# Kernel tuning notes

Measured on AMD Instinct MI355X. Metric: run time of the kernel, lower is better.

## Reference

```python
import jax, jax.numpy as jnp
import numpy as np

B, L, DM = 1, 512, 768
DS, DC, EX = 64, 4, 2
DI = EX * DM            # d_inner = 1536
DR = DM // 16           # dt_rank = 48


def setup_inputs() -> dict:
    key = jax.random.key(0)
    ks = jax.random.split(key, 12)
    s = 0.02
    inp = {
        "x": jax.random.normal(ks[0], (B, L, DM), dtype=jnp.float32),
        "ln_w": jnp.ones((DM,), jnp.float32),
        "ln_b": jnp.zeros((DM,), jnp.float32),
        "in_proj_w": jax.random.normal(ks[1], (2 * DI, DM), jnp.float32) * s,
        "conv_w": jax.random.normal(ks[2], (DI, 1, DC), jnp.float32) * s,
        "conv_b": jnp.zeros((DI,), jnp.float32),
        "x_proj_w": jax.random.normal(ks[3], (DR + 2 * DS, DI), jnp.float32) * s,
        "dt_proj_w": jax.random.normal(ks[4], (DI, DR), jnp.float32) * s,
        "dt_proj_b": jax.random.normal(ks[5], (DI,), jnp.float32) * s,
        "A_log": jnp.log(jnp.broadcast_to(jnp.arange(1, DS + 1, dtype=jnp.float32), (DI, DS))),
        "D": jnp.ones((DI,), jnp.float32),
        "out_proj_w": jax.random.normal(ks[6], (DM, DI), jnp.float32) * s,
    }
    return inp


def _layernorm(x, w, b, eps=1e-5):
    mu = jnp.mean(x, axis=-1, keepdims=True)
    var = jnp.mean((x - mu) ** 2, axis=-1, keepdims=True)
    return (x - mu) * jax.lax.rsqrt(var + eps) * w + b


def _causal_depthwise_conv(x, w, b):
    # x: [B, L, DI] -> conv over time, depthwise, causal (left pad DC-1)
    xc = jnp.transpose(x, (0, 2, 1))  # [B, DI, L]
    y = jax.lax.conv_general_dilated(
        xc, w, window_strides=(1,), padding=[(DC - 1, 0)],
        dimension_numbers=("NCH", "OIH", "NCH"), feature_group_count=DI)
    y = y + b[None, :, None]
    return jnp.transpose(y, (0, 2, 1))  # [B, L, DI]


def _selective_scan(deltaA, deltaB_u, C):
    # deltaA, deltaB_u: [B, L, DI, DS]; C: [B, L, DS]
    dA = jnp.transpose(deltaA, (1, 0, 2, 3))
    dBu = jnp.transpose(deltaB_u, (1, 0, 2, 3))
    Ct = jnp.transpose(C, (1, 0, 2))
    s0 = jnp.zeros(deltaA.shape[:1] + deltaA.shape[2:], deltaA.dtype).transpose(0, 1, 2)
    s0 = jnp.zeros((deltaA.shape[0], deltaA.shape[2], deltaA.shape[3]), deltaA.dtype)

    def step(s, inp):
        dA_t, dBu_t, C_t = inp
        s = dA_t * s + dBu_t                      # [B, DI, DS]
        y = jnp.einsum("bdn,bn->bd", s, C_t)      # [B, DI]
        return s, y

    _, ys = jax.lax.scan(step, s0, (dA, dBu, Ct))
    return jnp.transpose(ys, (1, 0, 2))           # [B, L, DI]


def reference(x, ln_w, ln_b, in_proj_w, conv_w, conv_b, x_proj_w,
              dt_proj_w, dt_proj_b, A_log, D, out_proj_w):
    residual = x
    h = _layernorm(x, ln_w, ln_b)
    xz = jnp.einsum("bld,ed->ble", h, in_proj_w)  # [B, L, 2*DI]
    x_in, z = jnp.split(xz, 2, axis=-1)
    x_in = jax.nn.silu(_causal_depthwise_conv(x_in, conv_w, conv_b))
    x_dbl = jnp.einsum("bld,ed->ble", x_in, x_proj_w)  # [B, L, DR+2*DS]
    dt, Bm, Cm = jnp.split(x_dbl, [DR, DR + DS], axis=-1)
    dt = jax.nn.softplus(jnp.einsum("blr,dr->bld", dt, dt_proj_w) + dt_proj_b)  # [B,L,DI]
    A = -jnp.exp(A_log)                                 # [DI, DS]
    deltaA = jnp.exp(dt[..., None] * A)                 # [B, L, DI, DS]
    deltaB_u = dt[..., None] * Bm[:, :, None, :] * x_in[..., None]
    y = _selective_scan(deltaA, deltaB_u, Cm)           # [B, L, DI]
    y = y + x_in * D
    y = y * jax.nn.silu(z)
    out = jnp.einsum("bld,ed->ble", y, out_proj_w)      # [B, L, DM]
    return residual + out
```

## Files before the change

### kernel.cpp

```cpp
#include <hip/hip_runtime.h>
#include <hip/hip_bf16.h>
#include <math.h>

#define L_SEQ 512
#define DM 768
#define DI 1536
#define DS 64
#define DC 4
#define DR 48
#define NBC 128
#define NP2 (NBC + DI)
#define NC 8
#define TC 64

typedef __attribute__((ext_vector_type(8))) short short8;
typedef __attribute__((ext_vector_type(4))) float float4v;

#define J_LN 512
#define J_WI (2 * DI * DM / 1024)
#define J_WBC (NBC * DI / 1024)
#define J_WO (DM * DI / 1024)
#define J_WEFF ((DI / 64) * (DI / 64))
#define PREP_GRID (J_LN + J_WI + J_WBC + J_WO + J_WEFF)

__device__ __forceinline__ float bp_add(float p, int addr) {
  return p + __int_as_float(__builtin_amdgcn_ds_bpermute(addr, __float_as_int(p)));
}
__device__ __forceinline__ float lane_read(float v, int t) {
  return __int_as_float(__builtin_amdgcn_readlane(__float_as_int(v), t));
}
__device__ __forceinline__ short f2bf(float v) {
  __hip_bfloat16 h = __float2bfloat16(v);
  return *reinterpret_cast<short*>(&h);
}
__device__ __forceinline__ short8 cvt8f(const float* p, bool valid) {
  float4 u = *(const float4*)(p);
  float4 v = *(const float4*)(p + 4);
  short8 r;
  r[0] = f2bf(u.x); r[1] = f2bf(u.y); r[2] = f2bf(u.z); r[3] = f2bf(u.w);
  r[4] = f2bf(v.x); r[5] = f2bf(v.y); r[6] = f2bf(v.z); r[7] = f2bf(v.w);
  if (!valid) r = (short8)0;
  return r;
}
__device__ __forceinline__ void cvt_blk(const float* __restrict__ s,
                                        short* __restrict__ d, int b) {
  int i = b * 1024 + threadIdx.x * 4;
  float4 v = *(const float4*)(s + i);
  short4 o; o.x = f2bf(v.x); o.y = f2bf(v.y); o.z = f2bf(v.z); o.w = f2bf(v.w);
  *(short4*)(d + i) = o;
}

__device__ __forceinline__ float4v gemm32_core(
    const short* __restrict__ A, int lda, const short* __restrict__ B, int ldb,
    int K, int bx, int by, int lane, int w, float4v* red,
    int* prow, int* pcol) {
  int ks = K >> 2;
  int kbeg = w * ks;
  int fr = lane & 15, koff = (lane >> 4) * 8;
  int m0 = by * 32, n0 = bx * 32;
  const short* pA0 = A + (size_t)(m0 + fr) * lda + koff + kbeg;
  const short* pA1 = pA0 + (size_t)16 * lda;
  const short* pB0 = B + (size_t)(n0 + fr) * ldb + koff + kbeg;
  const short* pB1 = pB0 + (size_t)16 * ldb;
  float4v acc00 = (float4v){0.f,0.f,0.f,0.f}, acc01 = acc00;
  float4v acc10 = acc00, acc11 = acc00;
  short8 a0A = *(const short8*)(pA0);      short8 a1A = *(const short8*)(pA1);
  short8 b0A = *(const short8*)(pB0);      short8 b1A = *(const short8*)(pB1);
  short8 a0B = *(const short8*)(pA0 + 32); short8 a1B = *(const short8*)(pA1 + 32);
  short8 b0B = *(const short8*)(pB0 + 32); short8 b1B = *(const short8*)(pB1 + 32);
  for (int k0 = 0; k0 < ks; k0 += 64) {
    short8 ca0 = a0A, ca1 = a1A, cb0 = b0A, cb1 = b1A;
    short8 da0 = a0B, da1 = a1B, db0 = b0B, db1 = b1B;
    int nA = k0 + 64; if (nA >= ks) nA = 0;
    int nB = k0 + 96; if (nB >= ks) nB = 32;
    a0A = *(const short8*)(pA0 + nA); a1A = *(const short8*)(pA1 + nA);
    b0A = *(const short8*)(pB0 + nA); b1A = *(const short8*)(pB1 + nA);
    a0B = *(const short8*)(pA0 + nB); a1B = *(const short8*)(pA1 + nB);
    b0B = *(const short8*)(pB0 + nB); b1B = *(const short8*)(pB1 + nB);
    acc00 = __builtin_amdgcn_mfma_f32_16x16x32_bf16(ca0, cb0, acc00, 0, 0, 0);
    acc01 = __builtin_amdgcn_mfma_f32_16x16x32_bf16(ca0, cb1, acc01, 0, 0, 0);
    acc10 = __builtin_amdgcn_mfma_f32_16x16x32_bf16(ca1, cb0, acc10, 0, 0, 0);
    acc11 = __builtin_amdgcn_mfma_f32_16x16x32_bf16(ca1, cb1, acc11, 0, 0, 0);
    acc00 = __builtin_amdgcn_mfma_f32_16x16x32_bf16(da0, db0, acc00, 0, 0, 0);
    acc01 = __builtin_amdgcn_mfma_f32_16x16x32_bf16(da0, db1, acc01, 0, 0, 0);
    acc10 = __builtin_amdgcn_mfma_f32_16x16x32_bf16(da1, db0, acc10, 0, 0, 0);
    acc11 = __builtin_amdgcn_mfma_f32_16x16x32_bf16(da1, db1, acc11, 0, 0, 0);
  }
  red[(w * 4 + 0) * 64 + lane] = acc00;
  red[(w * 4 + 1) * 64 + lane] = acc01;
  red[(w * 4 + 2) * 64 + lane] = acc10;
  red[(w * 4 + 3) * 64 + lane] = acc11;
  __syncthreads();
  float4v v = red[(0 * 4 + w) * 64 + lane];
  v = v + red[(1 * 4 + w) * 64 + lane];
  v = v + red[(2 * 4 + w) * 64 + lane];
  v = v + red[(3 * 4 + w) * 64 + lane];
  int qi = w & 1, qj = w >> 1;
  *prow = m0 + qi * 16 + (lane >> 4) * 4;
  *pcol = n0 + qj * 16 + (lane & 15);
  return v;
}

__global__ __launch_bounds__(256) void prep(
    const float* __restrict__ x, const float* __restrict__ lnw,
    const float* __restrict__ lnb, short* __restrict__ h,
    const float* __restrict__ wi, short* __restrict__ wib,
    const float* __restrict__ wx, const float* __restrict__ wdt,
    short* __restrict__ wcomb, const float* __restrict__ wo,
    short* __restrict__ wob) {
  __shared__ float ls[4], ls2[4];
  int b = blockIdx.x;
  int tid = threadIdx.x, lane = tid & 63, w = tid >> 6;
  if (b < J_LN) {
    int l = b;
    const float* xr = x + l * DM;
    float s = 0.f, s2 = 0.f;
    for (int i = tid; i < DM; i += 256) { float t = xr[i]; s += t; s2 += t * t; }
#pragma unroll
    for (int off = 32; off; off >>= 1) { s += __shfl_xor(s, off); s2 += __shfl_xor(s2, off); }
    if (lane == 0) { ls[w] = s; ls2[w] = s2; }
    __syncthreads();
    s = ls[0] + ls[1] + ls[2] + ls[3];
    s2 = ls2[0] + ls2[1] + ls2[2] + ls2[3];
    float mean = s * (1.f / DM);
    float var = s2 * (1.f / DM) - mean * mean;
    float rstd = rsqrtf(var + 1e-5f);
    for (int i = tid; i < DM; i += 256)
      h[l * DM + i] = f2bf((xr[i] - mean) * rstd * lnw[i] + lnb[i]);
    return;
  }
  b -= J_LN;
  if (b < J_WI) { cvt_blk(wi, wib, b); return; }
  b -= J_WI;
  if (b < J_WBC) { cvt_blk(wx + DR * DI, wcomb, b); return; }
  b -= J_WBC;
  if (b < J_WO) { cvt_blk(wo, wob, b); return; }
  b -= J_WO;
  {
    int tm = b / (DI / 64), tn = b % (DI / 64);
    int qi = w & 1, qj = w >> 1;
    int m0 = tm * 64 + qi * 32, n0 = tn * 64 + qj * 32;
    int fr = lane & 15, koff = (lane >> 4) * 8;
    const float* pA0 = wdt + (size_t)(m0 + fr) * DR;
    const float* pA1 = pA0 + (size_t)16 * DR;
    float4v a00 = (float4v){0.f,0.f,0.f,0.f}, a01 = a00, a10 = a00, a11 = a00;
#pragma unroll
    for (int k0 = 0; k0 < 64; k0 += 32) {
      bool valid = (k0 + koff) < DR;
      int off = valid ? k0 + koff : 0;
      short8 fa0 = cvt8f(pA0 + off, valid);
      short8 fa1 = cvt8f(pA1 + off, valid);
      short8 fb0, fb1;
#pragma unroll
      for (int j = 0; j < 8; ++j) {
        int r = k0 + koff + j;
        fb0[j] = valid ? f2bf(wx[(size_t)r * DI + n0 + fr]) : (short)0;
        fb1[j] = valid ? f2bf(wx[(size_t)r * DI + n0 + 16 + fr]) : (short)0;
      }
      a00 = __builtin_amdgcn_mfma_f32_16x16x32_bf16(fa0, fb0, a00, 0, 0, 0);
      a01 = __builtin_amdgcn_mfma_f32_16x16x32_bf16(fa0, fb1, a01, 0, 0, 0);
      a10 = __builtin_amdgcn_mfma_f32_16x16x32_bf16(fa1, fb0, a10, 0, 0, 0);
      a11 = __builtin_amdgcn_mfma_f32_16x16x32_bf16(fa1, fb1, a11, 0, 0, 0);
    }
    int rb = (lane >> 4) * 4, cb = lane & 15;
#pragma unroll
    for (int r = 0; r < 4; ++r) {
      wcomb[(size_t)(NBC + m0 + rb + r) * DI + n0 + cb]      = f2bf(a00[r]);
      wcomb[(size_t)(NBC + m0 + rb + r) * DI + n0 + 16 + cb] = f2bf(a01[r]);
      wcomb[(size_t)(NBC + m0 + 16 + rb + r) * DI + n0 + cb]      = f2bf(a10[r]);
      wcomb[(size_t)(NBC + m0 + 16 + rb + r) * DI + n0 + 16 + cb] = f2bf(a11[r]);
    }
  }
}

__global__ __launch_bounds__(256) void k_inproj(const short* __restrict__ h,
                                                const short* __restrict__ wi,
                                                float* __restrict__ xz) {
  __shared__ float4v red[16 * 64];
  int lane = threadIdx.x & 63, w = threadIdx.x >> 6;
  int row, col;
  float4v v = gemm32_core(h, DM, wi, DM, DM, blockIdx.x, blockIdx.y,
                          lane, w, red, &row, &col);
#pragma unroll
  for (int r = 0; r < 4; ++r)
    xz[(size_t)(row + r) * (2 * DI) + col] = v[r];
}

__global__ __launch_bounds__(256) void conv_silu_kernel(const float* __restrict__ xz,
                                                        const float* __restrict__ cw,
                                                        const float* __restrict__ cb,
                                                        float* __restrict__ xc,
                                                        short* __restrict__ xcb) {
  int idx = blockIdx.x * 256 + threadIdx.x;
  int l = idx / DI, d = idx - l * DI;
  float acc = cb[d];
#pragma unroll
  for (int j = 0; j < DC; ++j) {
    int ll = l - (DC - 1) + j;
    if (ll >= 0) acc = fmaf(xz[(size_t)ll * (2 * DI) + d], cw[d * DC + j], acc);
  }
  float sig = 1.f / (1.f + __expf(-acc));
  float v = acc * sig;
  xc[idx] = v;
  xcb[idx] = f2bf(v);
}

__global__ __launch_bounds__(256) void k_proj2(const short* __restrict__ xc,
                                               const short* __restrict__ wcomb,
                                               float* __restrict__ xdblBC,
                                               float* __restrict__ dtb,
                                               const float* __restrict__ bias) {
  __shared__ float4v red[16 * 64];
  int lane = threadIdx.x & 63, w = threadIdx.x >> 6;
  int row, col;
  float4v v = gemm32_core(xc, DI, wcomb, DI, DI, blockIdx.x, blockIdx.y,
                          lane, w, red, &row, &col);
  if (col < NBC) {
#pragma unroll
    for (int r = 0; r < 4; ++r)
      xdblBC[(size_t)(row + r) * NBC + col] = v[r];
  } else {
    int d = col - NBC;
    float bi = bias[d];
#pragma unroll
    for (int r = 0; r < 4; ++r) {
      float t = v[r] + bi;
      t = (t > 20.f) ? t : log1pf(__expf(t));
      dtb[(size_t)(row + r) * DI + d] = t;
    }
  }
}

__global__ __launch_bounds__(256) void scan_p1(const float* __restrict__ dt,
                                               const float* __restrict__ xc,
                                               const float* __restrict__ xdblBC,
                                               const float* __restrict__ A_log,
                                               float* __restrict__ send,
                                               float* __restrict__ dts) {
  int lane = threadIdx.x & 63;
  int wid = threadIdx.x >> 6;
  int pair = blockIdx.x * 4 + wid;
  int c = __builtin_amdgcn_readfirstlane(pair / DI);
  int d = __builtin_amdgcn_readfirstlane(pair - (pair / DI) * DI);
  float A = -__expf(A_log[(size_t)d * DS + lane]);
  int l0 = c * TC;
  float dtv = dt[(size_t)(l0 + lane) * DI + d];
  float xv  = xc[(size_t)(l0 + lane) * DI + d];
  const float* pB = xdblBC + (size_t)l0 * NBC + lane;
  float s = 0.f;
#pragma unroll 8
  for (int t = 0; t < TC; ++t) {
    float dt_c = lane_read(dtv, t);
    float x_c  = lane_read(xv, t);
    float B_c  = pB[(size_t)t * NBC];
    float dA = __expf(dt_c * A);
    s = fmaf(dA, s, dt_c * x_c * B_c);
  }
  float dsum = dtv;
  dsum = bp_add(dsum, (lane ^ 1) << 2);  dsum = bp_add(dsum, (lane ^ 2) << 2);
  dsum = bp_add(dsum, (lane ^ 4) << 2);  dsum = bp_add(dsum, (lane ^ 8) << 2);
  dsum = bp_add(dsum, (lane ^ 16) << 2); dsum = bp_add(dsum, (lane ^ 32) << 2);
  send[((size_t)c * DI + d) * DS + lane] = s;
  if (lane == 0) dts[c * DI + d] = dsum;
}

__global__ __launch_bounds__(256) void scan_p3(const float* __restrict__ dt,
                                               const float* __restrict__ xc,
                                               const float* __restrict__ xdblBC,
                                               const float* __restrict__ A_log,
                                               const float* __restrict__ Dv,
                                               const float* __restrict__ xz,
                                               const float* __restrict__ send,
                                               const float* __restrict__ dts,
                                               short* __restrict__ y) {
  __shared__ float Pb[4][16][66];
  int lane = threadIdx.x & 63;
  int wid = threadIdx.x >> 6;
  int pair = blockIdx.x * 4 + wid;
  int c = __builtin_amdgcn_readfirstlane(pair / DI);
  int d = __builtin_amdgcn_readfirstlane(pair - (pair / DI) * DI);
  float A = -__expf(A_log[(size_t)d * DS + lane]);
  float Dd = Dv[d];
  int l0 = c * TC;
  float dtv = dt[(size_t)(l0 + lane) * DI + d];
  float xv  = xc[(size_t)(l0 + lane) * DI + d];
  float zv  = xz[(size_t)(l0 + lane) * (2 * DI) + DI + d];
  float s = 0.f;
  for (int cc = 0; cc < c; ++cc) {
    float P = __expf(A * dts[cc * DI + d]);
    s = fmaf(P, s, send[((size_t)cc * DI + d) * DS + lane]);
  }
  const float* pB = xdblBC + (size_t)l0 * NBC + lane;
  float yv = 0.f;
#pragma unroll
  for (int sb = 0; sb < 4; ++sb) {
    float P[16];
#pragma unroll
    for (int j = 0; j < 16; ++j) {
      int t = sb * 16 + j;
      float dt_c = lane_read(dtv, t);
      float x_c  = lane_read(xv, t);
      float B_c  = pB[(size_t)t * NBC];
      float C_c  = pB[(size_t)t * NBC + DS];
      float dA = __expf(dt_c * A);
      s = fmaf(dA, s, dt_c * x_c * B_c);
      P[j] = s * C_c;
    }
#pragma unroll
    for (int j = 0; j < 16; ++j) Pb[wid][j][lane] = P[j];
    int t4 = lane >> 2, q = lane & 3;
    const float* row = &Pb[wid][t4][q * 16];
    float part = 0.f;
#pragma unroll
    for (int k = 0; k < 8; ++k) {
      float2 v2 = *(const float2*)(row + 2 * k);
      part += v2.x + v2.y;
    }
    part = bp_add(part, (lane ^ 1) << 2);
    part = bp_add(part, (lane ^ 2) << 2);
    float got = __int_as_float(
        __builtin_amdgcn_ds_bpermute((lane & 15) << 4, __float_as_int(part)));
    yv = ((lane >> 4) == sb) ? got : yv;
  }
  float sig = 1.f / (1.f + __expf(-zv));
  y[(size_t)(l0 + lane) * DI + d] = f2bf((yv + xv * Dd) * (zv * sig));
}

__global__ __launch_bounds__(256) void k_outproj(const short* __restrict__ y,
                                                 const short* __restrict__ wo,
                                                 const float* __restrict__ x,
                                                 float* __restrict__ out) {
  __shared__ float4v red[16 * 64];
  int lane = threadIdx.x & 63, w = threadIdx.x >> 6;
  int row, col;
  float4v v = gemm32_core(y, DI, wo, DI, DI, blockIdx.x, blockIdx.y,
                          lane, w, red, &row, &col);
#pragma unroll
  for (int r = 0; r < 4; ++r)
    out[(size_t)(row + r) * DM + col] = v[r] + x[(size_t)(row + r) * DM + col];
}

extern "C" void kernel_launch(void* const* d_in, const int* in_sizes, int n_in,
                              void* d_out, int out_size, void* d_ws, size_t ws_size,
                              hipStream_t stream) {
  const float* x         = (const float*)d_in[0];
  const float* ln_w      = (const float*)d_in[1];
  const float* ln_b      = (const float*)d_in[2];
  const float* in_proj_w = (const float*)d_in[3];
  const float* conv_w    = (const float*)d_in[4];
  const float* conv_b    = (const float*)d_in[5];
  const float* x_proj_w  = (const float*)d_in[6];
  const float* dt_proj_w = (const float*)d_in[7];
  const float* dt_proj_b = (const float*)d_in[8];
  const float* A_log     = (const float*)d_in[9];
  const float* Dv        = (const float*)d_in[10];
  const float* out_proj_w= (const float*)d_in[11];
  float* out = (float*)d_out;

  float* ws = (float*)d_ws;
  float* xz     = ws;
  float* xconv  = xz + 1572864;
  float* xdblBC = xconv + 786432;
  float* dtb    = xdblBC + 65536;
  float* send   = dtb + 786432;
  float* dts    = send + 688128;
  float* fend   = dts + 10752;
  short* h_bf   = (short*)fend;
  short* wi_bf  = h_bf + 393216;
  short* wo_bf  = wi_bf + 2359296;
  short* wcomb  = wo_bf + 1179648;
  short* xc_bf  = wcomb + 2555904;
  short* y_bf   = xc_bf + 786432;

  prep<<<PREP_GRID, 256, 0, stream>>>(x, ln_w, ln_b, h_bf, in_proj_w, wi_bf,
                                      x_proj_w, dt_proj_w, wcomb,
                                      out_proj_w, wo_bf);

  k_inproj<<<dim3(2 * DI / 32, L_SEQ / 32), 256, 0, stream>>>(h_bf, wi_bf, xz);

  conv_silu_kernel<<<(L_SEQ * DI) / 256, 256, 0, stream>>>(xz, conv_w, conv_b,
                                                           xconv, xc_bf);

  k_proj2<<<dim3(NP2 / 32, L_SEQ / 32), 256, 0, stream>>>(
      xc_bf, wcomb, xdblBC, dtb, dt_proj_b);

  scan_p1<<<((NC - 1) * DI) / 4, 256, 0, stream>>>(dtb, xconv, xdblBC, A_log,
                                                   send, dts);
  scan_p3<<<(NC * DI) / 4, 256, 0, stream>>>(dtb, xconv, xdblBC, A_log, Dv, xz,
                                             send, dts, y_bf);

  k_outproj<<<dim3(DM / 32, L_SEQ / 32), 256, 0, stream>>>(y_bf, wo_bf, x, out);
}
```

Before: 205.0 us.

## Store scan inputs transposed per channel for coalesced scan loads

```diff
diff --git a/kernel.cpp b/kernel.cpp
--- a/kernel.cpp
+++ b/kernel.cpp
@@ -52,8 +52,7 @@
 
 __device__ __forceinline__ float4v gemm32_core(
     const short* __restrict__ A, int lda, const short* __restrict__ B, int ldb,
-    int K, int bx, int by, int lane, int w, float4v* red,
-    int* prow, int* pcol) {
+    int K, int bx, int by, int lane, int w, float4v* red) {
   int ks = K >> 2;
   int kbeg = w * ks;
   int fr = lane & 15, koff = (lane >> 4) * 8;
@@ -95,10 +94,20 @@
   v = v + red[(1 * 4 + w) * 64 + lane];
   v = v + red[(2 * 4 + w) * 64 + lane];
   v = v + red[(3 * 4 + w) * 64 + lane];
-  int qi = w & 1, qj = w >> 1;
-  *prow = m0 + qi * 16 + (lane >> 4) * 4;
-  *pcol = n0 + qj * 16 + (lane & 15);
   return v;
+}
+
+__device__ __forceinline__ void trans_store32(float* t, float4v v,
+                                              int lrow, int lcol, int tid,
+                                              float* dst, size_t ldT, int m0) {
+  __syncthreads();
+#pragma unroll
+  for (int r = 0; r < 4; ++r) t[lcol * 33 + lrow + r] = v[r];
+  __syncthreads();
+  int i = tid >> 3, j = (tid & 7) * 4;
+  float4 o = make_float4(t[i * 33 + j], t[i * 33 + j + 1],
+                         t[i * 33 + j + 2], t[i * 33 + j + 3]);
+  *(float4*)&dst[(size_t)i * ldT + m0 + j] = o;
 }
 
 __global__ __launch_bounds__(256) void prep(
@@ -175,64 +184,98 @@
 
 __global__ __launch_bounds__(256) void k_inproj(const short* __restrict__ h,
                                                 const short* __restrict__ wi,
-                                                float* __restrict__ xz) {
+                                                float* __restrict__ xz_in,
+                                                float* __restrict__ zt) {
   __shared__ float4v red[16 * 64];
-  int lane = threadIdx.x & 63, w = threadIdx.x >> 6;
-  int row, col;
-  float4v v = gemm32_core(h, DM, wi, DM, DM, blockIdx.x, blockIdx.y,
-                          lane, w, red, &row, &col);
-#pragma unroll
-  for (int r = 0; r < 4; ++r)
-    xz[(size_t)(row + r) * (2 * DI) + col] = v[r];
-}
-
-__global__ __launch_bounds__(256) void conv_silu_kernel(const float* __restrict__ xz,
+  int tid = threadIdx.x, lane = tid & 63, w = tid >> 6;
+  float4v v = gemm32_core(h, DM, wi, DM, DM, blockIdx.x, blockIdx.y, lane, w, red);
+  int lrow = ((w & 1) << 4) + ((lane >> 4) << 2);
+  int lcol = ((w >> 1) << 4) + (lane & 15);
+  int m0 = blockIdx.y * 32, n0 = blockIdx.x * 32;
+  if (n0 < DI) {
+#pragma unroll
+    for (int r = 0; r < 4; ++r)
+      xz_in[(size_t)(m0 + lrow + r) * DI + n0 + lcol] = v[r];
+  } else {
+    trans_store32((float*)red, v, lrow, lcol, tid,
+                  zt + (size_t)(n0 - DI) * L_SEQ, L_SEQ, m0);
+  }
+}
+
+__global__ __launch_bounds__(256) void conv_silu_kernel(const float* __restrict__ xz_in,
                                                         const float* __restrict__ cw,
                                                         const float* __restrict__ cb,
-                                                        float* __restrict__ xc,
-                                                        short* __restrict__ xcb) {
-  int idx = blockIdx.x * 256 + threadIdx.x;
-  int l = idx / DI, d = idx - l * DI;
-  float acc = cb[d];
-#pragma unroll
-  for (int j = 0; j < DC; ++j) {
-    int ll = l - (DC - 1) + j;
-    if (ll >= 0) acc = fmaf(xz[(size_t)ll * (2 * DI) + d], cw[d * DC + j], acc);
-  }
-  float sig = 1.f / (1.f + __expf(-acc));
-  float v = acc * sig;
-  xc[idx] = v;
-  xcb[idx] = f2bf(v);
+                                                        short* __restrict__ xc_bf,
+                                                        float* __restrict__ xct) {
+  __shared__ float t2[64 * 34];
+  int tid = threadIdx.x;
+  int dloc = tid & 63, lseg = tid >> 6;
+  int d0 = blockIdx.x * 64, l0 = blockIdx.y * 32;
+  int d = d0 + dloc;
+  int lb = l0 + lseg * 8;
+  float xin[11];
+#pragma unroll
+  for (int i = 0; i < 11; ++i) {
+    int l = lb - 3 + i;
+    xin[i] = (l >= 0) ? xz_in[(size_t)l * DI + d] : 0.f;
+  }
+  float w0 = cw[d * 4 + 0], w1 = cw[d * 4 + 1];
+  float w2 = cw[d * 4 + 2], w3 = cw[d * 4 + 3];
+  float bias = cb[d];
+#pragma unroll
+  for (int j = 0; j < 8; ++j) {
+    float acc = bias;
+    acc = fmaf(w0, xin[j], acc);
+    acc = fmaf(w1, xin[j + 1], acc);
+    acc = fmaf(w2, xin[j + 2], acc);
+    acc = fmaf(w3, xin[j + 3], acc);
+    float sig = 1.f / (1.f + __expf(-acc));
+    float v = acc * sig;
+    xc_bf[(size_t)(lb + j) * DI + d] = f2bf(v);
+    t2[dloc * 34 + lseg * 8 + j] = v;
+  }
+  __syncthreads();
+  int row = tid >> 2, j4 = (tid & 3) * 8;
+  const float* src = &t2[row * 34 + j4];
+  float2 o0 = *(const float2*)(src + 0);
+  float2 o1 = *(const float2*)(src + 2);
+  float2 o2 = *(const float2*)(src + 4);
+  float2 o3 = *(const float2*)(src + 6);
+  float* dst = &xct[(size_t)(d0 + row) * L_SEQ + l0 + j4];
+  *(float2*)(dst + 0) = o0; *(float2*)(dst + 2) = o1;
+  *(float2*)(dst + 4) = o2; *(float2*)(dst + 6) = o3;
 }
 
 __global__ __launch_bounds__(256) void k_proj2(const short* __restrict__ xc,
                                                const short* __restrict__ wcomb,
                                                float* __restrict__ xdblBC,
-                                               float* __restrict__ dtb,
+                                               float* __restrict__ dtt,
                                                const float* __restrict__ bias) {
   __shared__ float4v red[16 * 64];
-  int lane = threadIdx.x & 63, w = threadIdx.x >> 6;
-  int row, col;
+  int tid = threadIdx.x, lane = tid & 63, w = tid >> 6;
   float4v v = gemm32_core(xc, DI, wcomb, DI, DI, blockIdx.x, blockIdx.y,
-                          lane, w, red, &row, &col);
-  if (col < NBC) {
+                          lane, w, red);
+  int lrow = ((w & 1) << 4) + ((lane >> 4) << 2);
+  int lcol = ((w >> 1) << 4) + (lane & 15);
+  int m0 = blockIdx.y * 32, n0 = blockIdx.x * 32;
+  if (n0 < NBC) {
 #pragma unroll
     for (int r = 0; r < 4; ++r)
-      xdblBC[(size_t)(row + r) * NBC + col] = v[r];
+      xdblBC[(size_t)(m0 + lrow + r) * NBC + n0 + lcol] = v[r];
   } else {
-    int d = col - NBC;
-    float bi = bias[d];
+    float bi = bias[n0 - NBC + lcol];
 #pragma unroll
     for (int r = 0; r < 4; ++r) {
       float t = v[r] + bi;
-      t = (t > 20.f) ? t : log1pf(__expf(t));
-      dtb[(size_t)(row + r) * DI + d] = t;
+      v[r] = (t > 20.f) ? t : log1pf(__expf(t));
     }
-  }
-}
-
-__global__ __launch_bounds__(256) void scan_p1(const float* __restrict__ dt,
-                                               const float* __restrict__ xc,
+    trans_store32((float*)red, v, lrow, lcol, tid,
+                  dtt + (size_t)(n0 - NBC) * L_SEQ, L_SEQ, m0);
+  }
+}
+
+__global__ __launch_bounds__(256) void scan_p1(const float* __restrict__ dtt,
+                                               const float* __restrict__ xct,
                                                const float* __restrict__ xdblBC,
                                                const float* __restrict__ A_log,
                                                float* __restrict__ send,
@@ -244,8 +287,8 @@
   int d = __builtin_amdgcn_readfirstlane(pair - (pair / DI) * DI);
   float A = -__expf(A_log[(size_t)d * DS + lane]);
   int l0 = c * TC;
-  float dtv = dt[(size_t)(l0 + lane) * DI + d];
-  float xv  = xc[(size_t)(l0 + lane) * DI + d];
+  float dtv = dtt[(size_t)d * L_SEQ + l0 + lane];
+  float xv  = xct[(size_t)d * L_SEQ + l0 + lane];
   const float* pB = xdblBC + (size_t)l0 * NBC + lane;
   float s = 0.f;
 #pragma unroll 8
@@ -264,27 +307,29 @@
   if (lane == 0) dts[c * DI + d] = dsum;
 }
 
-__global__ __launch_bounds__(256) void scan_p3(const float* __restrict__ dt,
-                                               const float* __restrict__ xc,
+__global__ __launch_bounds__(256) void scan_p3(const float* __restrict__ dtt,
+                                               const float* __restrict__ xct,
                                                const float* __restrict__ xdblBC,
                                                const float* __restrict__ A_log,
                                                const float* __restrict__ Dv,
-                                               const float* __restrict__ xz,
+                                               const float* __restrict__ zt,
                                                const float* __restrict__ send,
                                                const float* __restrict__ dts,
                                                short* __restrict__ y) {
   __shared__ float Pb[4][16][66];
-  int lane = threadIdx.x & 63;
-  int wid = threadIdx.x >> 6;
+  __shared__ float ys[64][5];
+  int tid = threadIdx.x;
+  int lane = tid & 63;
+  int wid = tid >> 6;
   int pair = blockIdx.x * 4 + wid;
   int c = __builtin_amdgcn_readfirstlane(pair / DI);
   int d = __builtin_amdgcn_readfirstlane(pair - (pair / DI) * DI);
   float A = -__expf(A_log[(size_t)d * DS + lane]);
   float Dd = Dv[d];
   int l0 = c * TC;
-  float dtv = dt[(size_t)(l0 + lane) * DI + d];
-  float xv  = xc[(size_t)(l0 + lane) * DI + d];
-  float zv  = xz[(size_t)(l0 + lane) * (2 * DI) + DI + d];
+  float dtv = dtt[(size_t)d * L_SEQ + l0 + lane];
+  float xv  = xct[(size_t)d * L_SEQ + l0 + lane];
+  float zv  = zt[(size_t)d * L_SEQ + l0 + lane];
   float s = 0.f;
   for (int cc = 0; cc < c; ++cc) {
     float P = __expf(A * dts[cc * DI + d]);
@@ -323,7 +368,15 @@
     yv = ((lane >> 4) == sb) ? got : yv;
   }
   float sig = 1.f / (1.f + __expf(-zv));
-  y[(size_t)(l0 + lane) * DI + d] = f2bf((yv + xv * Dd) * (zv * sig));
+  ys[lane][wid] = (yv + xv * Dd) * (zv * sig);
+  __syncthreads();
+  if (tid < 64) {
+    int d0 = (blockIdx.x * 4) % DI;
+    short4 o;
+    o.x = f2bf(ys[tid][0]); o.y = f2bf(ys[tid][1]);
+    o.z = f2bf(ys[tid][2]); o.w = f2bf(ys[tid][3]);
+    *(short4*)&y[(size_t)(l0 + tid) * DI + d0] = o;
+  }
 }
 
 __global__ __launch_bounds__(256) void k_outproj(const short* __restrict__ y,
@@ -331,10 +384,11 @@
                                                  const float* __restrict__ x,
                                                  float* __restrict__ out) {
   __shared__ float4v red[16 * 64];
-  int lane = threadIdx.x & 63, w = threadIdx.x >> 6;
-  int row, col;
-  float4v v = gemm32_core(y, DI, wo, DI, DI, blockIdx.x, blockIdx.y,
-                          lane, w, red, &row, &col);
+  int tid = threadIdx.x, lane = tid & 63, w = tid >> 6;
+  float4v v = gemm32_core(y, DI, wo, DI, DI, blockIdx.x, blockIdx.y, lane, w, red);
+  int lrow = ((w & 1) << 4) + ((lane >> 4) << 2);
+  int lcol = ((w >> 1) << 4) + (lane & 15);
+  int row = blockIdx.y * 32 + lrow, col = blockIdx.x * 32 + lcol;
 #pragma unroll
   for (int r = 0; r < 4; ++r)
     out[(size_t)(row + r) * DM + col] = v[r] + x[(size_t)(row + r) * DM + col];
@@ -358,11 +412,12 @@
   float* out = (float*)d_out;
 
   float* ws = (float*)d_ws;
-  float* xz     = ws;
-  float* xconv  = xz + 1572864;
-  float* xdblBC = xconv + 786432;
-  float* dtb    = xdblBC + 65536;
-  float* send   = dtb + 786432;
+  float* xz_in  = ws;
+  float* zt     = xz_in + 786432;
+  float* xct    = zt + 786432;
+  float* dtt    = xct + 786432;
+  float* xdblBC = dtt + 786432;
+  float* send   = xdblBC + 65536;
   float* dts    = send + 688128;
   float* fend   = dts + 10752;
   short* h_bf   = (short*)fend;
@@ -376,17 +431,18 @@
                                       x_proj_w, dt_proj_w, wcomb,
                                       out_proj_w, wo_bf);
 
-  k_inproj<<<dim3(2 * DI / 32, L_SEQ / 32), 256, 0, stream>>>(h_bf, wi_bf, xz);
-
-  conv_silu_kernel<<<(L_SEQ * DI) / 256, 256, 0, stream>>>(xz, conv_w, conv_b,
-                                                           xconv, xc_bf);
+  k_inproj<<<dim3(2 * DI / 32, L_SEQ / 32), 256, 0, stream>>>(h_bf, wi_bf,
+                                                              xz_in, zt);
+
+  conv_silu_kernel<<<dim3(DI / 64, L_SEQ / 32), 256, 0, stream>>>(
+      xz_in, conv_w, conv_b, xc_bf, xct);
 
   k_proj2<<<dim3(NP2 / 32, L_SEQ / 32), 256, 0, stream>>>(
-      xc_bf, wcomb, xdblBC, dtb, dt_proj_b);
-
-  scan_p1<<<((NC - 1) * DI) / 4, 256, 0, stream>>>(dtb, xconv, xdblBC, A_log,
+      xc_bf, wcomb, xdblBC, dtt, dt_proj_b);
+
+  scan_p1<<<((NC - 1) * DI) / 4, 256, 0, stream>>>(dtt, xct, xdblBC, A_log,
                                                    send, dts);
-  scan_p3<<<(NC * DI) / 4, 256, 0, stream>>>(dtb, xconv, xdblBC, A_log, Dv, xz,
+  scan_p3<<<(NC * DI) / 4, 256, 0, stream>>>(dtt, xct, xdblBC, A_log, Dv, zt,
                                              send, dts, y_bf);
 
   k_outproj<<<dim3(DM / 32, L_SEQ / 32), 256, 0, stream>>>(y_bf, wo_bf, x, out);
```

Result: faster. 187.6 us (-8.5%).
